# Performance work log

Hardware: AMD Instinct MI355X
Metric: run time of the kernel (lower is better)

The kernel has to match this reference:

```python
import jax, jax.numpy as jnp
import numpy as np

N_COARSE = 100000
N_FINE = 400000
E = 1600000
C = 64


def setup_inputs() -> dict:
    key = jax.random.key(0)
    ks = jax.random.split(key, 9)
    x = jax.random.normal(ks[0], (N_COARSE, C), dtype=jnp.float32)
    W = jax.random.normal(ks[1], (C, C), dtype=jnp.float32) * (1.0 / np.sqrt(C))
    b = jax.random.normal(ks[2], (C,), dtype=jnp.float32) * 0.01
    edge_index = jax.random.randint(ks[3], (2, E), 0, N_COARSE, dtype=jnp.int64)
    edge_attr = jax.random.uniform(ks[4], (E,), dtype=jnp.float32)
    pool_src = jax.random.randint(ks[5], (E,), 0, N_COARSE, dtype=jnp.int64)
    pool_dst = jax.random.randint(ks[6], (E,), 0, N_FINE, dtype=jnp.int64)
    pool_edge_attr = jax.random.uniform(ks[7], (E,), dtype=jnp.float32)
    # direct-injection map: each coarse node has a unique fine-node slot
    pool_fwd_idx = jax.random.permutation(ks[8], N_FINE)[:N_COARSE].astype(jnp.int64)
    return {"x": x, "W": W, "b": b, "edge_index": edge_index,
            "edge_attr": edge_attr, "pool_src": pool_src, "pool_dst": pool_dst,
            "pool_edge_attr": pool_edge_attr, "pool_fwd_idx": pool_fwd_idx}


def reference(x, W, b, edge_index, edge_attr, pool_src, pool_dst,
              pool_edge_attr, pool_fwd_idx):
    # --- CustomGraphConvPointPoint: edge-weighted gather, scatter-add, linear ---
    src, dst = edge_index[0], edge_index[1]
    msgs = edge_attr[:, None] * x[src]                       # [E, C]
    agg = jax.ops.segment_sum(msgs, dst, num_segments=N_COARSE)  # [N_coarse, C]
    h = agg @ W + b                                          # [N_coarse, C]
    # --- CustomUnpooling: weighted prolongation to fine graph + direct copy ---
    pmsgs = pool_edge_attr[:, None] * h[pool_src]            # [E, C]
    out = jax.ops.segment_sum(pmsgs, pool_dst, num_segments=N_FINE)  # [N_fine, C]
    out = out.at[pool_fwd_idx].set(h)                        # inject coarse values
    return out
```

## Files before the change

kernel.cpp:

```cpp
#include <hip/hip_runtime.h>

#define NC 100000
#define NF 400000
#define NE 1600000
#define C  64


#define NSUB 512
#define CAPB 4096
#define SUBC 196
#define SUBF 782

template<int SUBDIV>
__global__ __launch_bounds__(256) void k_partition(
    const int* __restrict__ dst, const int* __restrict__ src,
    const float* __restrict__ w, int* __restrict__ cur, int2* __restrict__ buf)
{
    __shared__ int lcnt[NSUB];
    int tid = threadIdx.x;
    int e0 = blockIdx.x * 4096;
    for (int i = tid; i < NSUB; i += 256) lcnt[i] = 0;
    __syncthreads();
    int rb[16]; int2 rv[16];
    #pragma unroll
    for (int i = 0; i < 16; ++i) {
        int e = e0 + i * 256 + tid;
        if (e < NE) {
            int d  = dst[e];
            int bk = d / SUBDIV;
            rb[i]  = bk;
            rv[i]  = make_int2(((d - bk * SUBDIV) << 17) | src[e],
                               __float_as_int(w[e]));
            atomicAdd(&lcnt[bk], 1);
        } else rb[i] = -1;
    }
    __syncthreads();
    for (int i = tid; i < NSUB; i += 256)
        lcnt[i] = i * CAPB + atomicAdd(&cur[i], lcnt[i]);
    __syncthreads();
    #pragma unroll
    for (int i = 0; i < 16; ++i) {
        if (rb[i] >= 0) {
            int p = atomicAdd(&lcnt[rb[i]], 1);
            if (p < (rb[i] + 1) * CAPB) buf[p] = rv[i];
        }
    }
}

template<int SUBDIV, int NTOT, bool FINE>
__global__ __launch_bounds__(1024, 8) void k_sortgather(
    const int2* __restrict__ buf, const int* __restrict__ cur,
    const float* __restrict__ feat,
    const int* __restrict__ inv,
    float* __restrict__ outp)
{
    __shared__ int2 srt[CAPB];
    __shared__ int  cnt[SUBDIV];
    __shared__ int  scn[1024];
    int tid = threadIdx.x;
    int blk = blockIdx.x;
    int nodeLo = blk * SUBDIV;
    int nNodes = min(SUBDIV, NTOT - nodeLo);
    if (nNodes <= 0) return;
    int lo = blk * CAPB;
    int n  = min(cur[blk], CAPB);

    for (int i = tid; i < SUBDIV; i += 1024) cnt[i] = 0;
    __syncthreads();

    int2 r[CAPB / 1024];
    #pragma unroll
    for (int k = 0; k < CAPB / 1024; ++k) {
        int i = k * 1024 + tid;
        if (i < n) { r[k] = buf[lo + i]; atomicAdd(&cnt[r[k].x >> 17], 1); }
        else r[k].x = -1;
    }
    __syncthreads();

    int v = (tid < SUBDIV) ? cnt[tid] : 0;
    scn[tid] = v; __syncthreads();
    for (int off = 1; off < 1024; off <<= 1) {
        int x = scn[tid];
        if (tid >= off) x += scn[tid - off];
        __syncthreads(); scn[tid] = x; __syncthreads();
    }
    if (tid < SUBDIV) cnt[tid] = scn[tid] - v;
    __syncthreads();

    #pragma unroll
    for (int k = 0; k < CAPB / 1024; ++k) {
        if (r[k].x >= 0) {
            int p = atomicAdd(&cnt[r[k].x >> 17], 1);
            srt[p] = r[k];
        }
    }
    __syncthreads();

    int qd = tid >> 4;
    int c4 = (tid & 15) << 2;
    for (int nl = qd; nl < nNodes; nl += 64) {
        int node = nodeLo + nl;
        if (FINE) {
            int iv = inv[node];
            if (iv >= 0) {
                float4 vv = *(const float4*)(feat + (size_t)iv * C + c4);
                *(float4*)(outp + (size_t)node * C + c4) = vv;
                continue;
            }
        }
        int s = (nl == 0) ? 0 : cnt[nl - 1];
        int e = cnt[nl];
        float ax = 0.f, ay = 0.f, az = 0.f, aw = 0.f;
        for (int j = s; j < e; j += 4) {
            int2 q0 = srt[j];
            int2 q1 = (j + 1 < e) ? srt[j + 1] : make_int2(0, 0);
            int2 q2 = (j + 2 < e) ? srt[j + 2] : make_int2(0, 0);
            int2 q3 = (j + 3 < e) ? srt[j + 3] : make_int2(0, 0);
            float4 v0 = *(const float4*)(feat + (size_t)(q0.x & 0x1FFFF) * C + c4);
            float4 v1 = *(const float4*)(feat + (size_t)(q1.x & 0x1FFFF) * C + c4);
            float4 v2 = *(const float4*)(feat + (size_t)(q2.x & 0x1FFFF) * C + c4);
            float4 v3 = *(const float4*)(feat + (size_t)(q3.x & 0x1FFFF) * C + c4);
            float w0 = __int_as_float(q0.y), w1 = __int_as_float(q1.y);
            float w2 = __int_as_float(q2.y), w3 = __int_as_float(q3.y);
            ax = fmaf(w0, v0.x, ax); ay = fmaf(w0, v0.y, ay);
            az = fmaf(w0, v0.z, az); aw = fmaf(w0, v0.w, aw);
            ax = fmaf(w1, v1.x, ax); ay = fmaf(w1, v1.y, ay);
            az = fmaf(w1, v1.z, az); aw = fmaf(w1, v1.w, aw);
            ax = fmaf(w2, v2.x, ax); ay = fmaf(w2, v2.y, ay);
            az = fmaf(w2, v2.z, az); aw = fmaf(w2, v2.w, aw);
            ax = fmaf(w3, v3.x, ax); ay = fmaf(w3, v3.y, ay);
            az = fmaf(w3, v3.z, az); aw = fmaf(w3, v3.w, aw);
        }
        *(float4*)(outp + (size_t)node * C + c4) = make_float4(ax, ay, az, aw);
    }
}

__global__ __launch_bounds__(256, 1) void k_gemm_ip(
    float* __restrict__ h, const float* __restrict__ W, const float* __restrict__ b)
{
    int tid = threadIdx.x;
    int lane = tid & 63;
    float wreg[64];
    #pragma unroll
    for (int k = 0; k < 64; ++k) wreg[k] = W[k * C + lane];
    float bl = b[lane];
    int wv = (blockIdx.x * 256 + tid) >> 6;
    int nW = gridDim.x * 4;
    for (int row = wv; row < NC; row += 2 * nW) {
        int row2 = row + nW;
        bool has2 = row2 < NC;
        int row2c = has2 ? row2 : row;
        float* ar  = h + (size_t)row * C;
        float* ar2 = h + (size_t)row2c * C;
        float acc = bl, acc2 = bl;
        #pragma unroll
        for (int kk = 0; kk < 16; ++kk) {
            float4 a4 = *(const float4*)(ar + 4 * kk);
            float4 b4 = *(const float4*)(ar2 + 4 * kk);
            acc  = fmaf(a4.x, wreg[4 * kk + 0], acc);
            acc  = fmaf(a4.y, wreg[4 * kk + 1], acc);
            acc  = fmaf(a4.z, wreg[4 * kk + 2], acc);
            acc  = fmaf(a4.w, wreg[4 * kk + 3], acc);
            acc2 = fmaf(b4.x, wreg[4 * kk + 0], acc2);
            acc2 = fmaf(b4.y, wreg[4 * kk + 1], acc2);
            acc2 = fmaf(b4.z, wreg[4 * kk + 2], acc2);
            acc2 = fmaf(b4.w, wreg[4 * kk + 3], acc2);
        }
        ar[lane] = acc;
        if (has2) ar2[lane] = acc2;
    }
}

__global__ __launch_bounds__(256) void k_inv(
    const int* __restrict__ fwd, int* __restrict__ inv, int* __restrict__ cur)
{
    int i = blockIdx.x * 256 + threadIdx.x;
    if (i < NC) inv[fwd[i]] = i;
    if (blockIdx.x == 0)
        for (int j = threadIdx.x; j < 2 * NSUB; j += 256) cur[j] = 0;
}

extern "C" void kernel_launch(void* const* d_in, const int* in_sizes, int n_in,
                              void* d_out, int out_size, void* d_ws, size_t ws_size,
                              hipStream_t stream) {
    const float* x    = (const float*)d_in[0];
    const float* W    = (const float*)d_in[1];
    const float* b    = (const float*)d_in[2];
    const int*   ei   = (const int*)d_in[3];
    const float* ea   = (const float*)d_in[4];
    const int*   psrc = (const int*)d_in[5];
    const int*   pdst = (const int*)d_in[6];
    const float* pw   = (const float*)d_in[7];
    const int*   fwd  = (const int*)d_in[8];
    float* out = (float*)d_out;

    char* p = (char*)d_ws;
    float* h   = (float*)p;  p += (size_t)NC * C * sizeof(float);
    int2*  buf = (int2*)p;   p += (size_t)NSUB * CAPB * sizeof(int2);
    int*   inv = (int*)p;    p += (size_t)NF * sizeof(int);
    int*   curC = (int*)p;   p += NSUB * sizeof(int);
    int*   curF = (int*)p;   p += NSUB * sizeof(int);

    const int nTiles = (NE + 4095) / 4096;

    hipMemsetAsync(inv, 0xFF, (size_t)NF * sizeof(int), stream);
    k_inv<<<(NC + 255) / 256, 256, 0, stream>>>(fwd, inv, curC);

    k_partition<SUBC><<<nTiles, 256, 0, stream>>>(ei + NE, ei, ea, curC, buf);
    k_sortgather<SUBC, NC, false><<<NSUB, 1024, 0, stream>>>(
        buf, curC, x, nullptr, h);
    k_gemm_ip<<<2048, 256, 0, stream>>>(h, W, b);

    k_partition<SUBF><<<nTiles, 256, 0, stream>>>(pdst, psrc, pw, curF, buf);
    k_sortgather<SUBF, NF, true><<<NSUB, 1024, 0, stream>>>(
        buf, curF, h, inv, out);
}
```

Before: 363.5 us.

## Fuse linear layer into coarse sortgather and locally sort partition writes

The 64x64 linear layer plus bias moves into the coarse aggregation kernel. W is staged in LDS and each node's aggregated row is exchanged across its 16-lane quad with shuffles, so h is written only once and never re-read. The separate GEMM launch and its read-modify-write of h go away. The partition kernel now sorts edges by bucket in shared memory before scattering, so global writes to each bucket are contiguous rather than randomly interleaved. This costs extra LDS, a scan and more ALU and shuffle work in the gather epilogue, which may lower occupancy.

New measurement: 758.4 us. 109% more time.

```diff
diff --git a/kernel.cpp b/kernel.cpp
--- a/kernel.cpp
+++ b/kernel.cpp
@@ -16,11 +16,18 @@
     const int* __restrict__ dst, const int* __restrict__ src,
     const float* __restrict__ w, int* __restrict__ cur, int2* __restrict__ buf)
 {
-    __shared__ int lcnt[NSUB];
+    __shared__ int2 srt[4096];
+    __shared__ unsigned short bkl[4096];
+    __shared__ int cnt[NSUB];
+    __shared__ int excl[NSUB];
+    __shared__ int cur2[NSUB];
+    __shared__ int resv[NSUB];
+    __shared__ int psum[256];
     int tid = threadIdx.x;
     int e0 = blockIdx.x * 4096;
-    for (int i = tid; i < NSUB; i += 256) lcnt[i] = 0;
-    __syncthreads();
+    for (int i = tid; i < NSUB; i += 256) cnt[i] = 0;
+    __syncthreads();
+
     int rb[16]; int2 rv[16];
     #pragma unroll
     for (int i = 0; i < 16; ++i) {
@@ -31,32 +38,59 @@
             rb[i]  = bk;
             rv[i]  = make_int2(((d - bk * SUBDIV) << 17) | src[e],
                                __float_as_int(w[e]));
-            atomicAdd(&lcnt[bk], 1);
+            atomicAdd(&cnt[bk], 1);
         } else rb[i] = -1;
     }
     __syncthreads();
-    for (int i = tid; i < NSUB; i += 256)
-        lcnt[i] = i * CAPB + atomicAdd(&cur[i], lcnt[i]);
-    __syncthreads();
+
+    int c0 = cnt[2 * tid], c1 = cnt[2 * tid + 1];
+    psum[tid] = c0 + c1;
+    __syncthreads();
+    for (int off = 1; off < 256; off <<= 1) {
+        int v = psum[tid];
+        if (tid >= off) v += psum[tid - off];
+        __syncthreads(); psum[tid] = v; __syncthreads();
+    }
+    int base = psum[tid] - (c0 + c1);
+    excl[2 * tid]     = base;
+    excl[2 * tid + 1] = base + c0;
+    cur2[2 * tid]     = base;
+    cur2[2 * tid + 1] = base + c0;
+    resv[2 * tid]     = (2 * tid) * CAPB     + atomicAdd(&cur[2 * tid], c0);
+    resv[2 * tid + 1] = (2 * tid + 1) * CAPB + atomicAdd(&cur[2 * tid + 1], c1);
+    __syncthreads();
+
     #pragma unroll
     for (int i = 0; i < 16; ++i) {
         if (rb[i] >= 0) {
-            int p = atomicAdd(&lcnt[rb[i]], 1);
-            if (p < (rb[i] + 1) * CAPB) buf[p] = rv[i];
-        }
-    }
-}
-
-template<int SUBDIV, int NTOT, bool FINE>
+            int p = atomicAdd(&cur2[rb[i]], 1);
+            srt[p] = rv[i];
+            bkl[p] = (unsigned short)rb[i];
+        }
+    }
+    __syncthreads();
+
+    int n = min(NE - e0, 4096);
+    for (int i = tid; i < n; i += 256) {
+        int bk = bkl[i];
+        int g  = resv[bk] + (i - excl[bk]);
+        if (g < (bk + 1) * CAPB) buf[g] = srt[i];
+    }
+}
+
+template<int SUBDIV, int NTOT, bool FINE, bool GEMM>
 __global__ __launch_bounds__(1024, 8) void k_sortgather(
     const int2* __restrict__ buf, const int* __restrict__ cur,
     const float* __restrict__ feat,
     const int* __restrict__ inv,
+    const float* __restrict__ W,
+    const float* __restrict__ bias,
     float* __restrict__ outp)
 {
     __shared__ int2 srt[CAPB];
     __shared__ int  cnt[SUBDIV];
     __shared__ int  scn[1024];
+    __shared__ float Wl[GEMM ? 4096 : 4];
     int tid = threadIdx.x;
     int blk = blockIdx.x;
     int nodeLo = blk * SUBDIV;
@@ -65,6 +99,8 @@
     int lo = blk * CAPB;
     int n  = min(cur[blk], CAPB);
 
+    if (GEMM)
+        ((float4*)Wl)[tid] = ((const float4*)W)[tid];
     for (int i = tid; i < SUBDIV; i += 1024) cnt[i] = 0;
     __syncthreads();
 
@@ -97,7 +133,10 @@
     __syncthreads();
 
     int qd = tid >> 4;
-    int c4 = (tid & 15) << 2;
+    int ql = tid & 15;
+    int c4 = ql << 2;
+    int qbase = (tid & 63) & ~15;
+    float4 bv = GEMM ? ((const float4*)bias)[ql] : make_float4(0, 0, 0, 0);
     for (int nl = qd; nl < nNodes; nl += 64) {
         int node = nodeLo + nl;
         if (FINE) {
@@ -131,43 +170,33 @@
             ax = fmaf(w3, v3.x, ax); ay = fmaf(w3, v3.y, ay);
             az = fmaf(w3, v3.z, az); aw = fmaf(w3, v3.w, aw);
         }
-        *(float4*)(outp + (size_t)node * C + c4) = make_float4(ax, ay, az, aw);
-    }
-}
-
-__global__ __launch_bounds__(256, 1) void k_gemm_ip(
-    float* __restrict__ h, const float* __restrict__ W, const float* __restrict__ b)
-{
-    int tid = threadIdx.x;
-    int lane = tid & 63;
-    float wreg[64];
-    #pragma unroll
-    for (int k = 0; k < 64; ++k) wreg[k] = W[k * C + lane];
-    float bl = b[lane];
-    int wv = (blockIdx.x * 256 + tid) >> 6;
-    int nW = gridDim.x * 4;
-    for (int row = wv; row < NC; row += 2 * nW) {
-        int row2 = row + nW;
-        bool has2 = row2 < NC;
-        int row2c = has2 ? row2 : row;
-        float* ar  = h + (size_t)row * C;
-        float* ar2 = h + (size_t)row2c * C;
-        float acc = bl, acc2 = bl;
-        #pragma unroll
-        for (int kk = 0; kk < 16; ++kk) {
-            float4 a4 = *(const float4*)(ar + 4 * kk);
-            float4 b4 = *(const float4*)(ar2 + 4 * kk);
-            acc  = fmaf(a4.x, wreg[4 * kk + 0], acc);
-            acc  = fmaf(a4.y, wreg[4 * kk + 1], acc);
-            acc  = fmaf(a4.z, wreg[4 * kk + 2], acc);
-            acc  = fmaf(a4.w, wreg[4 * kk + 3], acc);
-            acc2 = fmaf(b4.x, wreg[4 * kk + 0], acc2);
-            acc2 = fmaf(b4.y, wreg[4 * kk + 1], acc2);
-            acc2 = fmaf(b4.z, wreg[4 * kk + 2], acc2);
-            acc2 = fmaf(b4.w, wreg[4 * kk + 3], acc2);
-        }
-        ar[lane] = acc;
-        if (has2) ar2[lane] = acc2;
+        if (!GEMM) {
+            *(float4*)(outp + (size_t)node * C + c4) =
+                make_float4(ax, ay, az, aw);
+        } else {
+            float h0 = bv.x, h1 = bv.y, h2 = bv.z, h3 = bv.w;
+            #pragma unroll
+            for (int jj = 0; jj < 16; ++jj) {
+                float r0 = __shfl(ax, qbase + jj);
+                float r1 = __shfl(ay, qbase + jj);
+                float r2 = __shfl(az, qbase + jj);
+                float r3 = __shfl(aw, qbase + jj);
+                float4 w0 = ((const float4*)Wl)[(4 * jj + 0) * 16 + ql];
+                float4 w1 = ((const float4*)Wl)[(4 * jj + 1) * 16 + ql];
+                float4 w2 = ((const float4*)Wl)[(4 * jj + 2) * 16 + ql];
+                float4 w3 = ((const float4*)Wl)[(4 * jj + 3) * 16 + ql];
+                h0 = fmaf(r0, w0.x, h0); h1 = fmaf(r0, w0.y, h1);
+                h2 = fmaf(r0, w0.z, h2); h3 = fmaf(r0, w0.w, h3);
+                h0 = fmaf(r1, w1.x, h0); h1 = fmaf(r1, w1.y, h1);
+                h2 = fmaf(r1, w1.z, h2); h3 = fmaf(r1, w1.w, h3);
+                h0 = fmaf(r2, w2.x, h0); h1 = fmaf(r2, w2.y, h1);
+                h2 = fmaf(r2, w2.z, h2); h3 = fmaf(r2, w2.w, h3);
+                h0 = fmaf(r3, w3.x, h0); h1 = fmaf(r3, w3.y, h1);
+                h2 = fmaf(r3, w3.z, h2); h3 = fmaf(r3, w3.w, h3);
+            }
+            *(float4*)(outp + (size_t)node * C + c4) =
+                make_float4(h0, h1, h2, h3);
+        }
     }
 }
 
@@ -207,11 +236,10 @@
     k_inv<<<(NC + 255) / 256, 256, 0, stream>>>(fwd, inv, curC);
 
     k_partition<SUBC><<<nTiles, 256, 0, stream>>>(ei + NE, ei, ea, curC, buf);
-    k_sortgather<SUBC, NC, false><<<NSUB, 1024, 0, stream>>>(
-        buf, curC, x, nullptr, h);
-    k_gemm_ip<<<2048, 256, 0, stream>>>(h, W, b);
+    k_sortgather<SUBC, NC, false, true><<<NSUB, 1024, 0, stream>>>(
+        buf, curC, x, nullptr, W, b, h);
 
     k_partition<SUBF><<<nTiles, 256, 0, stream>>>(pdst, psrc, pw, curF, buf);
-    k_sortgather<SUBF, NF, true><<<NSUB, 1024, 0, stream>>>(
-        buf, curF, h, inv, out);
-}
+    k_sortgather<SUBF, NF, true, false><<<NSUB, 1024, 0, stream>>>(
+        buf, curF, h, inv, nullptr, nullptr, out);
+}
```

## Stage partitioned edges in LDS by bucket before writing to global buffers

Applied to the files above, without the earlier changes.

The partition kernel now runs a block-local counting sort. It builds an exclusive scan of the per-bucket counts, places each edge into shared memory grouped by bucket, then has consecutive threads write contiguous runs to each bucket's global region. Before, each thread scattered its edge straight to global memory at an atomic-chosen slot. The goal is more coalesced global stores. In exchange the kernel uses more shared memory (about 40KB, which may lower occupancy) and adds a scan with several barriers.

Result: slower. 373.3 us (+2.7%).

```diff
diff --git a/kernel.cpp b/kernel.cpp
--- a/kernel.cpp
+++ b/kernel.cpp
@@ -16,11 +16,18 @@
     const int* __restrict__ dst, const int* __restrict__ src,
     const float* __restrict__ w, int* __restrict__ cur, int2* __restrict__ buf)
 {
-    __shared__ int lcnt[NSUB];
+    __shared__ int2 srt[4096];
+    __shared__ unsigned short bkl[4096];
+    __shared__ int cnt[NSUB];
+    __shared__ int excl[NSUB];
+    __shared__ int cur2[NSUB];
+    __shared__ int resv[NSUB];
+    __shared__ int psum[256];
     int tid = threadIdx.x;
     int e0 = blockIdx.x * 4096;
-    for (int i = tid; i < NSUB; i += 256) lcnt[i] = 0;
-    __syncthreads();
+    for (int i = tid; i < NSUB; i += 256) cnt[i] = 0;
+    __syncthreads();
+
     int rb[16]; int2 rv[16];
     #pragma unroll
     for (int i = 0; i < 16; ++i) {
@@ -31,19 +38,43 @@
             rb[i]  = bk;
             rv[i]  = make_int2(((d - bk * SUBDIV) << 17) | src[e],
                                __float_as_int(w[e]));
-            atomicAdd(&lcnt[bk], 1);
+            atomicAdd(&cnt[bk], 1);
         } else rb[i] = -1;
     }
     __syncthreads();
-    for (int i = tid; i < NSUB; i += 256)
-        lcnt[i] = i * CAPB + atomicAdd(&cur[i], lcnt[i]);
-    __syncthreads();
+
+    int c0 = cnt[2 * tid], c1 = cnt[2 * tid + 1];
+    psum[tid] = c0 + c1;
+    __syncthreads();
+    for (int off = 1; off < 256; off <<= 1) {
+        int v = psum[tid];
+        if (tid >= off) v += psum[tid - off];
+        __syncthreads(); psum[tid] = v; __syncthreads();
+    }
+    int base = psum[tid] - (c0 + c1);
+    excl[2 * tid]     = base;
+    excl[2 * tid + 1] = base + c0;
+    cur2[2 * tid]     = base;
+    cur2[2 * tid + 1] = base + c0;
+    resv[2 * tid]     = (2 * tid) * CAPB     + atomicAdd(&cur[2 * tid], c0);
+    resv[2 * tid + 1] = (2 * tid + 1) * CAPB + atomicAdd(&cur[2 * tid + 1], c1);
+    __syncthreads();
+
     #pragma unroll
     for (int i = 0; i < 16; ++i) {
         if (rb[i] >= 0) {
-            int p = atomicAdd(&lcnt[rb[i]], 1);
-            if (p < (rb[i] + 1) * CAPB) buf[p] = rv[i];
-        }
+            int p = atomicAdd(&cur2[rb[i]], 1);
+            srt[p] = rv[i];
+            bkl[p] = (unsigned short)rb[i];
+        }
+    }
+    __syncthreads();
+
+    int n = min(NE - e0, 4096);
+    for (int i = tid; i < n; i += 256) {
+        int bk = bkl[i];
+        int g  = resv[bk] + (i - excl[bk]);
+        if (g < (bk + 1) * CAPB) buf[g] = srt[i];
     }
 }
 
```

## Merge both edge partition passes into one launch and tile the dense GEMM

Applied to the files above, without the earlier changes.

The coarse-graph and prolongation edge partitioning now run in a single kernel launch, using separate bucket buffers so the fine partition no longer waits for the coarse gather and GEMM. The per-row GEMM that kept W in registers with one block per CU is replaced by a 64x64 shared-memory tiled GEMM that computes a 4x4 register tile per thread. The aim is to cut launch serialization, give the partition work more parallelism, and give the GEMM better occupancy. The cost is an extra bucket buffer in workspace and the shared-memory footprint of the GEMM.

New measurement: 351.3 us. 3.4% less time.

```diff
diff --git a/kernel.cpp b/kernel.cpp
--- a/kernel.cpp
+++ b/kernel.cpp
@@ -10,15 +10,16 @@
 #define CAPB 4096
 #define SUBC 196
 #define SUBF 782
+#define NTILES ((NE + 4095) / 4096)
 
 template<int SUBDIV>
-__global__ __launch_bounds__(256) void k_partition(
+__device__ __forceinline__ void part_tile(
     const int* __restrict__ dst, const int* __restrict__ src,
-    const float* __restrict__ w, int* __restrict__ cur, int2* __restrict__ buf)
-{
-    __shared__ int lcnt[NSUB];
+    const float* __restrict__ w, int* __restrict__ cur, int2* __restrict__ buf,
+    int tile, int* lcnt)
+{
     int tid = threadIdx.x;
-    int e0 = blockIdx.x * 4096;
+    int e0 = tile * 4096;
     for (int i = tid; i < NSUB; i += 256) lcnt[i] = 0;
     __syncthreads();
     int rb[16]; int2 rv[16];
@@ -45,6 +46,21 @@
             if (p < (rb[i] + 1) * CAPB) buf[p] = rv[i];
         }
     }
+}
+
+__global__ __launch_bounds__(256) void k_part2(
+    const int* __restrict__ cd, const int* __restrict__ cs,
+    const float* __restrict__ cw,
+    const int* __restrict__ pd, const int* __restrict__ ps,
+    const float* __restrict__ pw,
+    int* __restrict__ curC, int* __restrict__ curF,
+    int2* __restrict__ bufC, int2* __restrict__ bufF)
+{
+    __shared__ int lcnt[NSUB];
+    if (blockIdx.x < NTILES)
+        part_tile<SUBC>(cd, cs, cw, curC, bufC, blockIdx.x, lcnt);
+    else
+        part_tile<SUBF>(pd, ps, pw, curF, bufF, blockIdx.x - NTILES, lcnt);
 }
 
 template<int SUBDIV, int NTOT, bool FINE>
@@ -135,40 +151,84 @@
     }
 }
 
-__global__ __launch_bounds__(256, 1) void k_gemm_ip(
-    float* __restrict__ h, const float* __restrict__ W, const float* __restrict__ b)
-{
+__global__ __launch_bounds__(256) void k_gemm_tile(
+    float* __restrict__ h, const float* __restrict__ W,
+    const float* __restrict__ bias)
+{
+    __shared__ float xs[64][68];
+    __shared__ float ws[64][68];
+    __shared__ float bs[64];
     int tid = threadIdx.x;
-    int lane = tid & 63;
-    float wreg[64];
-    #pragma unroll
-    for (int k = 0; k < 64; ++k) wreg[k] = W[k * C + lane];
-    float bl = b[lane];
-    int wv = (blockIdx.x * 256 + tid) >> 6;
-    int nW = gridDim.x * 4;
-    for (int row = wv; row < NC; row += 2 * nW) {
-        int row2 = row + nW;
-        bool has2 = row2 < NC;
-        int row2c = has2 ? row2 : row;
-        float* ar  = h + (size_t)row * C;
-        float* ar2 = h + (size_t)row2c * C;
-        float acc = bl, acc2 = bl;
-        #pragma unroll
-        for (int kk = 0; kk < 16; ++kk) {
-            float4 a4 = *(const float4*)(ar + 4 * kk);
-            float4 b4 = *(const float4*)(ar2 + 4 * kk);
-            acc  = fmaf(a4.x, wreg[4 * kk + 0], acc);
-            acc  = fmaf(a4.y, wreg[4 * kk + 1], acc);
-            acc  = fmaf(a4.z, wreg[4 * kk + 2], acc);
-            acc  = fmaf(a4.w, wreg[4 * kk + 3], acc);
-            acc2 = fmaf(b4.x, wreg[4 * kk + 0], acc2);
-            acc2 = fmaf(b4.y, wreg[4 * kk + 1], acc2);
-            acc2 = fmaf(b4.z, wreg[4 * kk + 2], acc2);
-            acc2 = fmaf(b4.w, wreg[4 * kk + 3], acc2);
-        }
-        ar[lane] = acc;
-        if (has2) ar2[lane] = acc2;
-    }
+    int r0 = blockIdx.x * 64;
+
+    for (int i = tid; i < 1024; i += 256) {
+        int k = i >> 4, c = (i & 15) << 2;
+        *(float4*)&ws[k][c] = ((const float4*)W)[i];
+        int r = r0 + k;
+        float4 xv = (r < NC) ? *(const float4*)(h + (size_t)r * C + c)
+                             : make_float4(0, 0, 0, 0);
+        *(float4*)&xs[k][c] = xv;
+    }
+    if (tid < 64) bs[tid] = bias[tid];
+    __syncthreads();
+
+    int tr = tid >> 4;
+    int tc = tid & 15;
+    float4 a0 = make_float4(0, 0, 0, 0), a1 = a0, a2 = a0, a3 = a0;
+    #pragma unroll
+    for (int kk = 0; kk < 16; ++kk) {
+        int k = kk << 2;
+        float4 x0 = *(const float4*)&xs[tr * 4 + 0][k];
+        float4 x1 = *(const float4*)&xs[tr * 4 + 1][k];
+        float4 x2 = *(const float4*)&xs[tr * 4 + 2][k];
+        float4 x3 = *(const float4*)&xs[tr * 4 + 3][k];
+        float4 w0 = *(const float4*)&ws[k + 0][tc * 4];
+        float4 w1 = *(const float4*)&ws[k + 1][tc * 4];
+        float4 w2 = *(const float4*)&ws[k + 2][tc * 4];
+        float4 w3 = *(const float4*)&ws[k + 3][tc * 4];
+        a0.x = fmaf(x0.x, w0.x, a0.x); a0.y = fmaf(x0.x, w0.y, a0.y);
+        a0.z = fmaf(x0.x, w0.z, a0.z); a0.w = fmaf(x0.x, w0.w, a0.w);
+        a0.x = fmaf(x0.y, w1.x, a0.x); a0.y = fmaf(x0.y, w1.y, a0.y);
+        a0.z = fmaf(x0.y, w1.z, a0.z); a0.w = fmaf(x0.y, w1.w, a0.w);
+        a0.x = fmaf(x0.z, w2.x, a0.x); a0.y = fmaf(x0.z, w2.y, a0.y);
+        a0.z = fmaf(x0.z, w2.z, a0.z); a0.w = fmaf(x0.z, w2.w, a0.w);
+        a0.x = fmaf(x0.w, w3.x, a0.x); a0.y = fmaf(x0.w, w3.y, a0.y);
+        a0.z = fmaf(x0.w, w3.z, a0.z); a0.w = fmaf(x0.w, w3.w, a0.w);
+        a1.x = fmaf(x1.x, w0.x, a1.x); a1.y = fmaf(x1.x, w0.y, a1.y);
+        a1.z = fmaf(x1.x, w0.z, a1.z); a1.w = fmaf(x1.x, w0.w, a1.w);
+        a1.x = fmaf(x1.y, w1.x, a1.x); a1.y = fmaf(x1.y, w1.y, a1.y);
+        a1.z = fmaf(x1.y, w1.z, a1.z); a1.w = fmaf(x1.y, w1.w, a1.w);
+        a1.x = fmaf(x1.z, w2.x, a1.x); a1.y = fmaf(x1.z, w2.y, a1.y);
+        a1.z = fmaf(x1.z, w2.z, a1.z); a1.w = fmaf(x1.z, w2.w, a1.w);
+        a1.x = fmaf(x1.w, w3.x, a1.x); a1.y = fmaf(x1.w, w3.y, a1.y);
+        a1.z = fmaf(x1.w, w3.z, a1.z); a1.w = fmaf(x1.w, w3.w, a1.w);
+        a2.x = fmaf(x2.x, w0.x, a2.x); a2.y = fmaf(x2.x, w0.y, a2.y);
+        a2.z = fmaf(x2.x, w0.z, a2.z); a2.w = fmaf(x2.x, w0.w, a2.w);
+        a2.x = fmaf(x2.y, w1.x, a2.x); a2.y = fmaf(x2.y, w1.y, a2.y);
+        a2.z = fmaf(x2.y, w1.z, a2.z); a2.w = fmaf(x2.y, w1.w, a2.w);
+        a2.x = fmaf(x2.z, w2.x, a2.x); a2.y = fmaf(x2.z, w2.y, a2.y);
+        a2.z = fmaf(x2.z, w2.z, a2.z); a2.w = fmaf(x2.z, w2.w, a2.w);
+        a2.x = fmaf(x2.w, w3.x, a2.x); a2.y = fmaf(x2.w, w3.y, a2.y);
+        a2.z = fmaf(x2.w, w3.z, a2.z); a2.w = fmaf(x2.w, w3.w, a2.w);
+        a3.x = fmaf(x3.x, w0.x, a3.x); a3.y = fmaf(x3.x, w0.y, a3.y);
+        a3.z = fmaf(x3.x, w0.z, a3.z); a3.w = fmaf(x3.x, w0.w, a3.w);
+        a3.x = fmaf(x3.y, w1.x, a3.x); a3.y = fmaf(x3.y, w1.y, a3.y);
+        a3.z = fmaf(x3.y, w1.z, a3.z); a3.w = fmaf(x3.y, w1.w, a3.w);
+        a3.x = fmaf(x3.z, w2.x, a3.x); a3.y = fmaf(x3.z, w2.y, a3.y);
+        a3.z = fmaf(x3.z, w2.z, a3.z); a3.w = fmaf(x3.z, w2.w, a3.w);
+        a3.x = fmaf(x3.w, w3.x, a3.x); a3.y = fmaf(x3.w, w3.y, a3.y);
+        a3.z = fmaf(x3.w, w3.z, a3.z); a3.w = fmaf(x3.w, w3.w, a3.w);
+    }
+    float4 bv = *(const float4*)&bs[tc * 4];
+    a0.x += bv.x; a0.y += bv.y; a0.z += bv.z; a0.w += bv.w;
+    a1.x += bv.x; a1.y += bv.y; a1.z += bv.z; a1.w += bv.w;
+    a2.x += bv.x; a2.y += bv.y; a2.z += bv.z; a2.w += bv.w;
+    a3.x += bv.x; a3.y += bv.y; a3.z += bv.z; a3.w += bv.w;
+    int rb = r0 + tr * 4;
+    if (rb + 0 < NC) *(float4*)(h + (size_t)(rb + 0) * C + tc * 4) = a0;
+    if (rb + 1 < NC) *(float4*)(h + (size_t)(rb + 1) * C + tc * 4) = a1;
+    if (rb + 2 < NC) *(float4*)(h + (size_t)(rb + 2) * C + tc * 4) = a2;
+    if (rb + 3 < NC) *(float4*)(h + (size_t)(rb + 3) * C + tc * 4) = a3;
 }
 
 __global__ __launch_bounds__(256) void k_inv(
@@ -195,23 +255,23 @@
     float* out = (float*)d_out;
 
     char* p = (char*)d_ws;
-    float* h   = (float*)p;  p += (size_t)NC * C * sizeof(float);
-    int2*  buf = (int2*)p;   p += (size_t)NSUB * CAPB * sizeof(int2);
-    int*   inv = (int*)p;    p += (size_t)NF * sizeof(int);
-    int*   curC = (int*)p;   p += NSUB * sizeof(int);
-    int*   curF = (int*)p;   p += NSUB * sizeof(int);
-
-    const int nTiles = (NE + 4095) / 4096;
+    float* h    = (float*)p;  p += (size_t)NC * C * sizeof(float);
+    int2*  bufC = (int2*)p;   p += (size_t)NSUB * CAPB * sizeof(int2);
+    int2*  bufF = (int2*)p;   p += (size_t)NSUB * CAPB * sizeof(int2);
+    int*   inv  = (int*)p;    p += (size_t)NF * sizeof(int);
+    int*   curC = (int*)p;    p += NSUB * sizeof(int);
+    int*   curF = (int*)p;    p += NSUB * sizeof(int);
 
     hipMemsetAsync(inv, 0xFF, (size_t)NF * sizeof(int), stream);
     k_inv<<<(NC + 255) / 256, 256, 0, stream>>>(fwd, inv, curC);
 
-    k_partition<SUBC><<<nTiles, 256, 0, stream>>>(ei + NE, ei, ea, curC, buf);
+    k_part2<<<2 * NTILES, 256, 0, stream>>>(ei + NE, ei, ea, pdst, psrc, pw,
+                                            curC, curF, bufC, bufF);
+
     k_sortgather<SUBC, NC, false><<<NSUB, 1024, 0, stream>>>(
-        buf, curC, x, nullptr, h);
-    k_gemm_ip<<<2048, 256, 0, stream>>>(h, W, b);
-
-    k_partition<SUBF><<<nTiles, 256, 0, stream>>>(pdst, psrc, pw, curF, buf);
+        bufC, curC, x, nullptr, h);
+    k_gemm_tile<<<(NC + 63) / 64, 256, 0, stream>>>(h, W, b);
+
     k_sortgather<SUBF, NF, true><<<NSUB, 1024, 0, stream>>>(
-        buf, curF, h, inv, out);
-}
+        bufF, curF, h, inv, out);
+}
```
